# Performance work log

Hardware: AMD Instinct MI355X
Metric: run time of the kernel (lower is better)

## Reference

```python
import jax, jax.numpy as jnp
import numpy as np

B, DIM, WIDTH, DD, C2 = 16384, 64, 256, 64, 16
TRIL = jnp.tril_indices(DIM, -1)


def _lin_init(key, out_size, in_size, bias=True):
    lim = 1.0 / np.sqrt(in_size)
    kW, kb = jax.random.split(key)
    W = jax.random.uniform(kW, (out_size, in_size), jnp.float32, -lim, lim)
    if bias:
        return W, jax.random.uniform(kb, (out_size,), jnp.float32, -lim, lim)
    return W


def setup_inputs() -> dict:
    key = jax.random.key(0)
    ks = jax.random.split(key, 16)
    inp = {"t": jnp.zeros((1,), jnp.float32),
           "y": jax.random.normal(ks[0], (B, DIM), jnp.float32)}
    specs = [("energy", 1, 1), ("entropy", 1, 4), ("pA", DIM * (DIM - 1) // 2, 7),
             ("fC", DD * C2, 10), ("fB", DD * DIM, 13)]
    for name, out, i in specs:
        W0, b0 = _lin_init(ks[i], WIDTH, DIM)
        W1, b1 = _lin_init(ks[i + 1], WIDTH, WIDTH)
        W2 = _lin_init(ks[i + 2], out, WIDTH, bias=False)
        inp[name + "_W0"], inp[name + "_b0"] = W0, b0
        inp[name + "_W1"], inp[name + "_b1"] = W1, b1
        inp[name + "_W2"] = W2
    return inp


def _mlp(x, W0, b0, W1, b1, W2):
    # eqx.nn.MLP, depth=2, tanh activations, no final bias
    h = jnp.tanh(x @ W0.T + b0)
    h = jnp.tanh(h @ W1.T + b1)
    return h @ W2.T


def _grad_scalar(y, W0, b0, W1, b1, W2):
    # per-sample gradient of scalar MLP (energy/entropy)
    def f(yv):
        h = jnp.tanh(W0 @ yv + b0)
        h = jnp.tanh(W1 @ h + b1)
        return (W2 @ h)[0]
    return jax.vmap(jax.grad(f))(y)


def _poisson(A_flat, dE, dS):
    b = dE.shape[0]
    Amat = jnp.zeros((b, DIM, DIM), dE.dtype).at[:, TRIL[0], TRIL[1]].set(A_flat)
    A = Amat - jnp.swapaxes(Amat, 1, 2)  # antisymmetric
    AdE = jnp.einsum('bij,bj->bi', A, dE)
    AdS = jnp.einsum('bij,bj->bi', A, dS)
    dE_AdS = jnp.sum(dE * AdS, axis=-1, keepdims=True)
    dE_dS = jnp.sum(dE * dS, axis=-1, keepdims=True)
    dS_sq = jnp.sum(dS ** 2, axis=-1, keepdims=True)
    return AdE + (dE_AdS * dS - dE_dS * AdS) / dS_sq


def _friction(C, Bm, dE, dS):
    Dmat = jnp.einsum('bik,bjk->bij', C, C)  # (b, DD, DD)
    BdotdE = jnp.einsum('bij,bj->bi', Bm, dE)
    BdotdS = jnp.einsum('bij,bj->bi', Bm, dS)
    dE_sq = jnp.sum(dE ** 2, axis=-1, keepdims=True)  # (b,1)
    BdE = Bm - BdotdE[:, :, None] * dE[:, None, :] / dE_sq[:, None, :]
    dEdS = jnp.sum(dE * dS, axis=-1, keepdims=True)
    BdEdS = BdotdS - BdotdE * (dEdS / dE_sq)  # (b, DD)
    return jnp.einsum('bik,bkl,bi->bl', jnp.swapaxes(BdE, 1, 2), Dmat, BdEdS)


def reference(t, y,
              energy_W0, energy_b0, energy_W1, energy_b1, energy_W2,
              entropy_W0, entropy_b0, entropy_W1, entropy_b1, entropy_W2,
              pA_W0, pA_b0, pA_W1, pA_b1, pA_W2,
              fC_W0, fC_b0, fC_W1, fC_b1, fC_W2,
              fB_W0, fB_b0, fB_W1, fB_b1, fB_W2):
    b = y.shape[0]
    dE = _grad_scalar(y, energy_W0, energy_b0, energy_W1, energy_b1, energy_W2)
    dS = _grad_scalar(y, entropy_W0, entropy_b0, entropy_W1, entropy_b1, entropy_W2)
    A_flat = _mlp(y, pA_W0, pA_b0, pA_W1, pA_b1, pA_W2)
    C = _mlp(y, fC_W0, fC_b0, fC_W1, fC_b1, fC_W2).reshape(b, DD, C2)
    Bm = _mlp(y, fB_W0, fB_b0, fB_W1, fB_b1, fB_W2).reshape(b, DD, DIM)
    return _poisson(A_flat, dE, dS) + _friction(C, Bm, dE, dS)
```

## Files before the change

kernel.cpp:

```cpp
#include <hip/hip_runtime.h>
#include <math.h>

#define SB 16

#define OFF_W0T  0
#define OFF_W1T  81920
#define OFF_W2PT 409600
#define OFF_W2CT 925696
#define OFF_W2BT 1187840
#define OFF_DE   2236416
#define OFF_DS   3284992
#define WS_FLOATS 4337600
#define NPACK  1048576
#define NPACKC 262144
#define NPACKP 524288
#define WS3_FLOATS (WS_FLOATS + NPACK + NPACKC + NPACKP)
#define NK1 327680
#define WS4_FLOATS (WS3_FLOATS + NK1)
#define NK3F 163840
#define WS5_FLOATS (WS4_FLOATS + NK3F)
#define NK2F 81920
#define WS6_FLOATS (WS5_FLOATS + NK2F)

typedef __attribute__((ext_vector_type(8))) short bf16x8;
typedef __attribute__((ext_vector_type(4))) float f32x4;

__device__ __forceinline__ float4 f4fma(float a, float4 w, float4 c) {
    c.x = fmaf(a, w.x, c.x); c.y = fmaf(a, w.y, c.y);
    c.z = fmaf(a, w.z, c.z); c.w = fmaf(a, w.w, c.w);
    return c;
}

__device__ __forceinline__ float4 tanh4b(float4 a, float b) {
    return make_float4(tanhf(a.x + b), tanhf(a.y + b), tanhf(a.z + b), tanhf(a.w + b));
}

__device__ __forceinline__ void bf16split(float x, unsigned short& hi, unsigned short& lo) {
    unsigned b = __float_as_uint(x);
    unsigned h = (b + 0x7FFFu + ((b >> 16) & 1u)) >> 16;
    hi = (unsigned short)h;
    float r = x - __uint_as_float(h << 16);
    unsigned rb = __float_as_uint(r);
    lo = (unsigned short)((rb + 0x7FFFu + ((rb >> 16) & 1u)) >> 16);
}

#define MFMA3(acc, Ah, Al, Bh, Bl)                                            \
    acc = __builtin_amdgcn_mfma_f32_16x16x32_bf16(Ah, Bh, acc, 0, 0, 0);      \
    acc = __builtin_amdgcn_mfma_f32_16x16x32_bf16(Al, Bh, acc, 0, 0, 0);      \
    acc = __builtin_amdgcn_mfma_f32_16x16x32_bf16(Ah, Bl, acc, 0, 0, 0);

__global__ __launch_bounds__(1024) void k_transpose_all(
    float* __restrict__ ws, int skipmid,
    const float* __restrict__ W0a, const float* __restrict__ W0b, const float* __restrict__ W0c,
    const float* __restrict__ W0d, const float* __restrict__ W0e,
    const float* __restrict__ W1a, const float* __restrict__ W1b, const float* __restrict__ W1c,
    const float* __restrict__ W1d, const float* __restrict__ W1e,
    const float* __restrict__ W2p, const float* __restrict__ W2c, const float* __restrict__ W2b)
{
    int t = blockIdx.x * blockDim.x + threadIdx.x;
    if (t >= 2236416) {
        int e = t - 2236416;
        unsigned short* PK = (unsigned short*)(ws + WS_FLOATS);
        if (e < NPACK) {
            int j = e & 7, lane = (e >> 3) & 63, c = (e >> 9) & 7, tt = e >> 12;
            int k = c * 32 + ((lane >> 4) & 3) * 8 + j;
            int n = tt * 16 + (lane & 15);
            unsigned short hi, lo;
            bf16split(W2b[n * 256 + k], hi, lo);
            PK[e] = hi; PK[NPACK + e] = lo;
        } else if (e < NPACK + NPACKC) {
            int e2 = e - NPACK;
            unsigned short* PC = PK + 2 * NPACK;
            int j = e2 & 7, lane = (e2 >> 3) & 63, c = (e2 >> 9) & 7, tt = e2 >> 12;
            int k = c * 32 + ((lane >> 4) & 3) * 8 + j;
            int n = tt * 16 + (lane & 15);
            unsigned short hi, lo;
            bf16split(W2c[n * 256 + k], hi, lo);
            PC[e2] = hi; PC[NPACKC + e2] = lo;
        } else if (e < NPACK + NPACKC + NPACKP) {
            int e2 = e - NPACK - NPACKC;
            unsigned short* PP = PK + 2 * NPACK + 2 * NPACKC;
            int j = e2 & 7, lane = (e2 >> 3) & 63, c = (e2 >> 9) & 7, tt = e2 >> 12;
            int k = c * 32 + ((lane >> 4) & 3) * 8 + j;
            int n = tt * 16 + (lane & 15);
            float v = (n < 2016) ? W2p[n * 256 + k] : 0.f;
            unsigned short hi, lo;
            bf16split(v, hi, lo);
            PP[e2] = hi; PP[NPACKP + e2] = lo;
        } else if (e < NPACK + NPACKC + NPACKP + NK1) {
            int e2 = e - NPACK - NPACKC - NPACKP;
            unsigned short* PQ = PK + 2 * (NPACK + NPACKC + NPACKP);
            int net = e2 / 163840;
            int r = e2 - net * 163840;
            const float* W0m = net ? W0b : W0a;
            const float* W1m = net ? W1b : W1a;
            float v;
            if (r < 16384) {
                int j = r & 7, lane = (r >> 3) & 63, cb = (r >> 9) & 1, tt = r >> 10;
                int k = cb * 32 + ((lane >> 4) & 3) * 8 + j;
                int n = tt * 16 + (lane & 15);
                v = W0m[n * 64 + k];
            } else if (r < 81920) {
                int r2 = r - 16384;
                int j = r2 & 7, lane = (r2 >> 3) & 63, cb = (r2 >> 9) & 7, tt = r2 >> 12;
                int k = cb * 32 + ((lane >> 4) & 3) * 8 + j;
                int n = tt * 16 + (lane & 15);
                v = W1m[n * 256 + k];
            } else if (r < 147456) {
                int r2 = r - 81920;
                int j = r2 & 7, lane = (r2 >> 3) & 63, cb = (r2 >> 9) & 7, tt = r2 >> 12;
                int k = cb * 32 + ((lane >> 4) & 3) * 8 + j;
                int n = tt * 16 + (lane & 15);
                v = W1m[k * 256 + n];
            } else {
                int r2 = r - 147456;
                int j = r2 & 7, lane = (r2 >> 3) & 63, cb = (r2 >> 9) & 7, tt = r2 >> 12;
                int k = cb * 32 + ((lane >> 4) & 3) * 8 + j;
                int n = tt * 16 + (lane & 15);
                v = W0m[k * 64 + n];
            }
            unsigned short hi, lo;
            bf16split(v, hi, lo);
            PQ[e2] = hi; PQ[NK1 + e2] = lo;
        } else if (e < NPACK + NPACKC + NPACKP + NK1 + NK3F) {
            int e2 = e - NPACK - NPACKC - NPACKP - NK1;
            unsigned short* PQ = PK + 2 * (NPACK + NPACKC + NPACKP + NK1);
            int net = e2 / 81920;
            int r = e2 - net * 81920;
            const float* W0m = net ? W0e : W0d;
            const float* W1m = net ? W1e : W1d;
            float v;
            if (r < 16384) {
                int j = r & 7, lane = (r >> 3) & 63, cb = (r >> 9) & 1, tt = r >> 10;
                int k = cb * 32 + ((lane >> 4) & 3) * 8 + j;
                int n = tt * 16 + (lane & 15);
                v = W0m[n * 64 + k];
            } else {
                int r2 = r - 16384;
                int j = r2 & 7, lane = (r2 >> 3) & 63, cb = (r2 >> 9) & 7, tt = r2 >> 12;
                int k = cb * 32 + ((lane >> 4) & 3) * 8 + j;
                int n = tt * 16 + (lane & 15);
                v = W1m[n * 256 + k];
            }
            unsigned short hi, lo;
            bf16split(v, hi, lo);
            PQ[e2] = hi; PQ[NK3F + e2] = lo;
        } else if (e < NPACK + NPACKC + NPACKP + NK1 + NK3F + NK2F) {
            int r = e - NPACK - NPACKC - NPACKP - NK1 - NK3F;
            unsigned short* PQ = PK + 2 * (NPACK + NPACKC + NPACKP + NK1 + NK3F);
            float v;
            if (r < 16384) {
                int j = r & 7, lane = (r >> 3) & 63, cb = (r >> 9) & 1, tt = r >> 10;
                int k = cb * 32 + ((lane >> 4) & 3) * 8 + j;
                int n = tt * 16 + (lane & 15);
                v = W0c[n * 64 + k];
            } else {
                int r2 = r - 16384;
                int j = r2 & 7, lane = (r2 >> 3) & 63, cb = (r2 >> 9) & 7, tt = r2 >> 12;
                int k = cb * 32 + ((lane >> 4) & 3) * 8 + j;
                int n = tt * 16 + (lane & 15);
                v = W1c[n * 256 + k];
            }
            unsigned short hi, lo;
            bf16split(v, hi, lo);
            PQ[r] = hi; PQ[NK2F + r] = lo;
        }
        return;
    }
    if (skipmid && t >= 409600) return;
    const float* in;
    int o, R, C;
    float* out;
    if (t < 81920) {
        int m = t >> 14; o = t & 16383;
        const float* W0s[5] = {W0a, W0b, W0c, W0d, W0e};
        in = W0s[m]; out = ws + OFF_W0T + m * 16384; R = 256; C = 64;
    } else if (t < 409600) {
        int t2 = t - 81920;
        int m = t2 >> 16; o = t2 & 65535;
        const float* W1s[5] = {W1a, W1b, W1c, W1d, W1e};
        in = W1s[m]; out = ws + OFF_W1T + m * 65536; R = 256; C = 256;
    } else if (t < 925696) {
        o = t - 409600; in = W2p; out = ws + OFF_W2PT; R = 2016; C = 256;
    } else if (t < 1187840) {
        o = t - 925696; in = W2c; out = ws + OFF_W2CT; R = 1024; C = 256;
    } else {
        o = t - 1187840; in = W2b; out = ws + OFF_W2BT; R = 4096; C = 256;
    }
    int c = o / R, r = o - c * R;
    out[o] = in[r * C + c];
}

__global__ __launch_bounds__(1024, 2) void k1_grads_mf(
    const float* __restrict__ y, const float* __restrict__ ws,
    const float* __restrict__ b0E, const float* __restrict__ b1E, const float* __restrict__ w2E,
    const float* __restrict__ b0S, const float* __restrict__ b1S, const float* __restrict__ w2S,
    float* __restrict__ odE, float* __restrict__ odS)
{
    __shared__ float sH1f[4352];
    __shared__ unsigned short yAh[1024], yAl[1024];
    __shared__ unsigned short bAh[4096], bAl[4096];
    __shared__ unsigned short bBh[4096], bBl[4096];
    __shared__ float sPart[4352];

    const int tid = threadIdx.x;
    const int sbase = blockIdx.x * SB;
    const int wv = tid >> 6, l = tid & 63;

    {
        int s = tid >> 6, k = tid & 63;
        unsigned short hi, lo;
        bf16split(y[sbase * 64 + tid], hi, lo);
        int addr = ((k >> 5) * 64 + (s | (((k >> 3) & 3) << 4))) * 8 + (k & 7);
        yAh[addr] = hi; yAl[addr] = lo;
    }
    __syncthreads();

    const unsigned short* K1H = (const unsigned short*)(ws + WS3_FLOATS);
    const unsigned short* K1L = K1H + NK1;

    for (int m = 0; m < 2; ++m) {
        const float* b0 = m ? b0S : b0E;
        const float* b1 = m ? b1S : b1E;
        const float* w2 = m ? w2S : w2E;
        float* outg = m ? odS : odE;
        const int pbase = m * 163840;

        {
            const unsigned short* PH = K1H + pbase;
            const unsigned short* PL = K1L + pbase;
            f32x4 acc = {0.f, 0.f, 0.f, 0.f};
            #pragma unroll
            for (int cb = 0; cb < 2; ++cb) {
                bf16x8 Ah = *(const bf16x8*)(yAh + (cb * 64 + l) * 8);
                bf16x8 Al = *(const bf16x8*)(yAl + (cb * 64 + l) * 8);
                bf16x8 Bh = *(const bf16x8*)(PH + ((wv * 2 + cb) * 64 + l) * 8);
                bf16x8 Bl = *(const bf16x8*)(PL + ((wv * 2 + cb) * 64 + l) * 8);
                MFMA3(acc, Ah, Al, Bh, Bl);
            }
            int c = 16 * wv + (l & 15);
            float bb = b0[c];
            const int cblk = c >> 5, j0 = c & 7;
            const int lb2 = ((c >> 3) & 3) << 4;
            #pragma unroll
            for (int r = 0; r < 4; ++r) {
                int s = (l >> 4) * 4 + r;
                float h1 = tanhf(acc[r] + bb);
                sH1f[c * 17 + s] = h1;
                unsigned short hi, lo;
                bf16split(h1, hi, lo);
                int base = (cblk * 64 + (s | lb2)) * 8 + j0;
                bBh[base] = hi; bBl[base] = lo;
            }
        }
        __syncthreads();

        {
            const unsigned short* PH = K1H + pbase + 16384;
            const unsigned short* PL = K1L + pbase + 16384;
            f32x4 acc = {0.f, 0.f, 0.f, 0.f};
            #pragma unroll 1
            for (int cb = 0; cb < 8; ++cb) {
                bf16x8 Ah = *(const bf16x8*)(bBh + (cb * 64 + l) * 8);
                bf16x8 Al = *(const bf16x8*)(bBl + (cb * 64 + l) * 8);
                bf16x8 Bh = *(const bf16x8*)(PH + ((wv * 8 + cb) * 64 + l) * 8);
                bf16x8 Bl = *(const bf16x8*)(PL + ((wv * 8 + cb) * 64 + l) * 8);
                MFMA3(acc, Ah, Al, Bh, Bl);
            }
            int c = 16 * wv + (l & 15);
            float bb = b1[c], wvv = w2[c];
            const int cblk = c >> 5, j0 = c & 7;
            const int lb2 = ((c >> 3) & 3) << 4;
            #pragma unroll
            for (int r = 0; r < 4; ++r) {
                int s = (l >> 4) * 4 + r;
                float h2 = tanhf(acc[r] + bb);
                float g2 = (1.f - h2 * h2) * wvv;
                unsigned short hi, lo;
                bf16split(g2, hi, lo);
                int base = (cblk * 64 + (s | lb2)) * 8 + j0;
                bAh[base] = hi; bAl[base] = lo;
            }
        }
        __syncthreads();

        {
            const unsigned short* PH = K1H + pbase + 81920;
            const unsigned short* PL = K1L + pbase + 81920;
            f32x4 acc = {0.f, 0.f, 0.f, 0.f};
            #pragma unroll 1
            for (int cb = 0; cb < 8; ++cb) {
                bf16x8 Ah = *(const bf16x8*)(bAh + (cb * 64 + l) * 8);
                bf16x8 Al = *(const bf16x8*)(bAl + (cb * 64 + l) * 8);
                bf16x8 Bh = *(const bf16x8*)(PH + ((wv * 8 + cb) * 64 + l) * 8);
                bf16x8 Bl = *(const bf16x8*)(PL + ((wv * 8 + cb) * 64 + l) * 8);
                MFMA3(acc, Ah, Al, Bh, Bl);
            }
            int c = 16 * wv + (l & 15);
            const int cblk = c >> 5, j0 = c & 7;
            const int lb2 = ((c >> 3) & 3) << 4;
            #pragma unroll
            for (int r = 0; r < 4; ++r) {
                int s = (l >> 4) * 4 + r;
                float h1 = sH1f[c * 17 + s];
                float g1 = (1.f - h1 * h1) * acc[r];
                unsigned short hi, lo;
                bf16split(g1, hi, lo);
                int base = (cblk * 64 + (s | lb2)) * 8 + j0;
                bBh[base] = hi; bBl[base] = lo;
            }
        }
        __syncthreads();

        {
            const unsigned short* PH = K1H + pbase + 147456;
            const unsigned short* PL = K1L + pbase + 147456;
            const int t = wv & 3, kh = wv >> 2;
            f32x4 acc = {0.f, 0.f, 0.f, 0.f};
            #pragma unroll
            for (int q = 0; q < 2; ++q) {
                int cb = 2 * kh + q;
                bf16x8 Ah = *(const bf16x8*)(bBh + (cb * 64 + l) * 8);
                bf16x8 Al = *(const bf16x8*)(bBl + (cb * 64 + l) * 8);
                bf16x8 Bh = *(const bf16x8*)(PH + ((t * 8 + cb) * 64 + l) * 8);
                bf16x8 Bl = *(const bf16x8*)(PL + ((t * 8 + cb) * 64 + l) * 8);
                MFMA3(acc, Ah, Al, Bh, Bl);
            }
            #pragma unroll
            for (int r = 0; r < 4; ++r)
                sPart[(kh * 4 + t) * 272 + (l & 15) * 17 + ((l >> 4) * 4 + r)] = acc[r];
        }
        __syncthreads();
        {
            int s = tid >> 6, i = tid & 63;
            float v = 0.f;
            #pragma unroll
            for (int kh = 0; kh < 4; ++kh)
                v += sPart[(kh * 4 + (i >> 4)) * 272 + (i & 15) * 17 + s];
            outg[sbase * 64 + tid] = v;
        }
        __syncthreads();
    }
}

__global__ __launch_bounds__(1024, 4) void k2_poisson_mf(
    const float* __restrict__ y, const float* __restrict__ ws,
    const float* __restrict__ b0P, const float* __restrict__ b1P,
    float* __restrict__ dout)
{
    extern __shared__ float smem[];
    float* sa   = smem;
    unsigned short* sAh = (unsigned short*)(smem + 32384);
    unsigned short* sAl = (unsigned short*)(smem + 34432);
    float* sdE  = smem + 36480;
    float* sdS  = sdE + 1024;
    float* sH1T = sa;
    float* syT  = sa + 4096;

    const int tid = threadIdx.x;
    const int sbase = blockIdx.x * SB;
    const float* gdE = ws + OFF_DE;
    const float* gdS = ws + OFF_DS;

    {
        int s = tid >> 6, i = tid & 63;
        syT[i * 16 + s] = y[sbase * 64 + tid];
        sdE[tid] = gdE[sbase * 64 + tid];
        sdS[tid] = gdS[sbase * 64 + tid];
    }
    __syncthreads();

    const int c  = tid & 255;
    const int sg = tid >> 8;
    const int s4 = sg * 4;

    {
        const float* w0t = ws + OFF_W0T + 2 * 16384;
        float4 acc = {0, 0, 0, 0};
        #pragma unroll 4
        for (int k = 0; k < 64; ++k) {
            float w = w0t[k * 256 + c];
            float4 yv = *(const float4*)(syT + k * 16 + s4);
            acc = f4fma(w, yv, acc);
        }
        *(float4*)(sH1T + c * 16 + s4) = tanh4b(acc, b0P[c]);
    }
    __syncthreads();

    {
        const float* w1t = ws + OFF_W1T + 2 * 65536;
        float4 acc = {0, 0, 0, 0};
        #pragma unroll 4
        for (int k = 0; k < 256; ++k) {
            float w = w1t[k * 256 + c];
            float4 hv = *(const float4*)(sH1T + k * 16 + s4);
            acc = f4fma(w, hv, acc);
        }
        float4 h2 = tanh4b(acc, b1P[c]);
        const int cblk = c >> 5, j0 = c & 7;
        const int lbase = ((c >> 3) & 3) << 4;
        float va[4] = {h2.x, h2.y, h2.z, h2.w};
        #pragma unroll
        for (int q = 0; q < 4; ++q) {
            int lb = ((s4 + q) & 15) | lbase;
            int base = (cblk * 64 + lb) * 8 + j0;
            unsigned short hi, lo;
            bf16split(va[q], hi, lo);
            sAh[base] = hi;
            sAl[base] = lo;
        }
    }
    __syncthreads();

    {
        const unsigned short* PP = (const unsigned short*)(ws + WS_FLOATS) + 2 * NPACK + 2 * NPACKC;
        const unsigned short* PH = PP;
        const unsigned short* PL = PP + NPACKP;
        const int wv = tid >> 6, l = tid & 63;
        f32x4 accp[8];
        #pragma unroll
        for (int t0 = 0; t0 < 8; ++t0) accp[t0] = (f32x4){0.f, 0.f, 0.f, 0.f};
        #pragma unroll 1
        for (int cb = 0; cb < 8; ++cb) {
            bf16x8 Ah = *(const bf16x8*)(sAh + (cb * 64 + l) * 8);
            bf16x8 Al = *(const bf16x8*)(sAl + (cb * 64 + l) * 8);
            #pragma unroll
            for (int t0 = 0; t0 < 8; ++t0) {
                int t = 8 * wv + t0;
                bf16x8 Bh = *(const bf16x8*)(PH + ((t * 8 + cb) * 64 + l) * 8);
                bf16x8 Bl = *(const bf16x8*)(PL + ((t * 8 + cb) * 64 + l) * 8);
                MFMA3(accp[t0], Ah, Al, Bh, Bl);
            }
        }
        #pragma unroll
        for (int t0 = 0; t0 < 8; ++t0) {
            int n = (8 * wv + t0) * 16 + (l & 15);
            if (n < 2016) {
                #pragma unroll
                for (int r = 0; r < 4; ++r)
                    sa[((l >> 4) * 4 + r) * 2024 + n] = accp[t0][r];
            }
        }
    }
    __syncthreads();

    {
        const int s = tid >> 6;
        const int i = tid & 63;
        const int ib = i * (i - 1) / 2;
        const float* ap = sa + s * 2024;
        const float* dep = sdE + s * 64;
        const float* dsp = sdS + s * 64;

        float adE = 0.f, adS = 0.f;
        int trij = 0;
        #pragma unroll 4
        for (int j = 0; j < 64; ++j) {
            int t = (j < i) ? (ib + j) : (trij + i);
            float sel = (j < i) ? 1.f : ((j == i) ? 0.f : -1.f);
            float cc = sel * ap[t];
            adE = fmaf(cc, dep[j], adE);
            adS = fmaf(cc, dsp[j], adS);
            trij += j;
        }

        float de = dep[i], dsv = dsp[i];
        float p0 = de * adS;
        float p1 = de * dsv;
        float p2 = dsv * dsv;
        #pragma unroll
        for (int m = 1; m <= 32; m <<= 1) {
            p0 += __shfl_xor(p0, m);
            p1 += __shfl_xor(p1, m);
            p2 += __shfl_xor(p2, m);
        }
        float inv = 1.f / p2;
        dout[sbase * 64 + tid] = adE + (p0 * dsv - p1 * adS) * inv;
    }
}

__global__ __launch_bounds__(1024, 4) void k2_poisson_mf2(
    const float* __restrict__ y, const float* __restrict__ ws,
    const float* __restrict__ b0P, const float* __restrict__ b1P,
    float* __restrict__ dout)
{
    extern __shared__ float smem[];
    float* sa   = smem;
    unsigned short* yAh = (unsigned short*)(smem);
    unsigned short* yAl = (unsigned short*)(smem + 512);
    unsigned short* h1H = (unsigned short*)(smem + 1024);
    unsigned short* h1L = (unsigned short*)(smem + 3072);
    unsigned short* sAh = (unsigned short*)(smem + 32384);
    unsigned short* sAl = (unsigned short*)(smem + 34432);
    float* sdE  = smem + 36480;
    float* sdS  = sdE + 1024;

    const int tid = threadIdx.x;
    const int sbase = blockIdx.x * SB;
    const float* gdE = ws + OFF_DE;
    const float* gdS = ws + OFF_DS;

    {
        int s = tid >> 6, k = tid & 63;
        unsigned short hi, lo;
        bf16split(y[sbase * 64 + tid], hi, lo);
        int addr = ((k >> 5) * 64 + (s | (((k >> 3) & 3) << 4))) * 8 + (k & 7);
        yAh[addr] = hi; yAl[addr] = lo;
        sdE[tid] = gdE[sbase * 64 + tid];
        sdS[tid] = gdS[sbase * 64 + tid];
    }
    __syncthreads();

    const int wv = tid >> 6, l = tid & 63;
    const unsigned short* F2H = (const unsigned short*)(ws + WS5_FLOATS);
    const unsigned short* F2L = F2H + NK2F;

    {
        f32x4 acc = {0.f, 0.f, 0.f, 0.f};
        #pragma unroll
        for (int cb = 0; cb < 2; ++cb) {
            bf16x8 Ah = *(const bf16x8*)(yAh + (cb * 64 + l) * 8);
            bf16x8 Al = *(const bf16x8*)(yAl + (cb * 64 + l) * 8);
            bf16x8 Bh = *(const bf16x8*)(F2H + ((wv * 2 + cb) * 64 + l) * 8);
            bf16x8 Bl = *(const bf16x8*)(F2L + ((wv * 2 + cb) * 64 + l) * 8);
            MFMA3(acc, Ah, Al, Bh, Bl);
        }
        int c = 16 * wv + (l & 15);
        float bb = b0P[c];
        const int cblk = c >> 5, j0 = c & 7;
        const int lb2 = ((c >> 3) & 3) << 4;
        #pragma unroll
        for (int r = 0; r < 4; ++r) {
            int s = (l >> 4) * 4 + r;
            float h1 = tanhf(acc[r] + bb);
            unsigned short hi, lo;
            bf16split(h1, hi, lo);
            int base = (cblk * 64 + (s | lb2)) * 8 + j0;
            h1H[base] = hi; h1L[base] = lo;
        }
    }
    __syncthreads();

    {
        f32x4 acc = {0.f, 0.f, 0.f, 0.f};
        #pragma unroll 1
        for (int cb = 0; cb < 8; ++cb) {
            bf16x8 Ah = *(const bf16x8*)(h1H + (cb * 64 + l) * 8);
            bf16x8 Al = *(const bf16x8*)(h1L + (cb * 64 + l) * 8);
            bf16x8 Bh = *(const bf16x8*)(F2H + 16384 + ((wv * 8 + cb) * 64 + l) * 8);
            bf16x8 Bl = *(const bf16x8*)(F2L + 16384 + ((wv * 8 + cb) * 64 + l) * 8);
            MFMA3(acc, Ah, Al, Bh, Bl);
        }
        int c = 16 * wv + (l & 15);
        float bb = b1P[c];
        const int cblk = c >> 5, j0 = c & 7;
        const int lb2 = ((c >> 3) & 3) << 4;
        #pragma unroll
        for (int r = 0; r < 4; ++r) {
            int s = (l >> 4) * 4 + r;
            float h2 = tanhf(acc[r] + bb);
            unsigned short hi, lo;
            bf16split(h2, hi, lo);
            int base = (cblk * 64 + (s | lb2)) * 8 + j0;
            sAh[base] = hi; sAl[base] = lo;
        }
    }
    __syncthreads();

    {
        const unsigned short* PP = (const unsigned short*)(ws + WS_FLOATS) + 2 * NPACK + 2 * NPACKC;
        const unsigned short* PH = PP;
        const unsigned short* PL = PP + NPACKP;
        f32x4 accp[8];
        #pragma unroll
        for (int t0 = 0; t0 < 8; ++t0) accp[t0] = (f32x4){0.f, 0.f, 0.f, 0.f};
        #pragma unroll 1
        for (int cb = 0; cb < 8; ++cb) {
            bf16x8 Ah = *(const bf16x8*)(sAh + (cb * 64 + l) * 8);
            bf16x8 Al = *(const bf16x8*)(sAl + (cb * 64 + l) * 8);
            #pragma unroll
            for (int t0 = 0; t0 < 8; ++t0) {
                int t = 8 * wv + t0;
                bf16x8 Bh = *(const bf16x8*)(PH + ((t * 8 + cb) * 64 + l) * 8);
                bf16x8 Bl = *(const bf16x8*)(PL + ((t * 8 + cb) * 64 + l) * 8);
                MFMA3(accp[t0], Ah, Al, Bh, Bl);
            }
        }
        #pragma unroll
        for (int t0 = 0; t0 < 8; ++t0) {
            int n = (8 * wv + t0) * 16 + (l & 15);
            if (n < 2016) {
                #pragma unroll
                for (int r = 0; r < 4; ++r)
                    sa[((l >> 4) * 4 + r) * 2024 + n] = accp[t0][r];
            }
        }
    }
    __syncthreads();

    {
        const int s = tid >> 6;
        const int i = tid & 63;
        const int ib = i * (i - 1) / 2;
        const float* ap = sa + s * 2024;
        const float* dep = sdE + s * 64;
        const float* dsp = sdS + s * 64;

        float adE = 0.f, adS = 0.f;
        int trij = 0;
        #pragma unroll 4
        for (int j = 0; j < 64; ++j) {
            int t = (j < i) ? (ib + j) : (trij + i);
            float sel = (j < i) ? 1.f : ((j == i) ? 0.f : -1.f);
            float cc = sel * ap[t];
            adE = fmaf(cc, dep[j], adE);
            adS = fmaf(cc, dsp[j], adS);
            trij += j;
        }

        float de = dep[i], dsv = dsp[i];
        float p0 = de * adS;
        float p1 = de * dsv;
        float p2 = dsv * dsv;
        #pragma unroll
        for (int m = 1; m <= 32; m <<= 1) {
            p0 += __shfl_xor(p0, m);
            p1 += __shfl_xor(p1, m);
            p2 += __shfl_xor(p2, m);
        }
        float inv = 1.f / p2;
        dout[sbase * 64 + tid] = adE + (p0 * dsv - p1 * adS) * inv;
    }
}

__global__ __launch_bounds__(1024, 4) void k3_friction_mf3(
    const float* __restrict__ y, const float* __restrict__ ws,
    const float* __restrict__ b0C, const float* __restrict__ b1C,
    const float* __restrict__ b0B, const float* __restrict__ b1B,
    float* __restrict__ dout)
{
    extern __shared__ float smem[];
    unsigned short* yAh = (unsigned short*)(smem);
    unsigned short* yAl = (unsigned short*)(smem + 512);
    unsigned short* sAhc = (unsigned short*)(smem + 1024);
    unsigned short* sAlc = (unsigned short*)(smem + 3072);
    unsigned short* sAhb = (unsigned short*)(smem + 5120);
    unsigned short* sAlb = (unsigned short*)(smem + 7168);
    unsigned short* h1ch = (unsigned short*)(smem + 9216);
    unsigned short* h1cl = (unsigned short*)(smem + 11264);
    unsigned short* h1bh = (unsigned short*)(smem + 13312);
    unsigned short* h1bl = (unsigned short*)(smem + 15360);
    float* sC   = smem + 9216;
    float* sdE  = smem + 26640;
    float* sdS  = smem + 27664;
    float* sBdE = smem + 28688;
    float* sBdS = smem + 29712;
    float* sv   = smem + 30736;
    float* sq   = smem + 31760;
    float* sScal= smem + 32784;
    float* sr   = smem + 32848;

    const int tid = threadIdx.x;
    const int sbase = blockIdx.x * SB;
    const float* gdE = ws + OFF_DE;
    const float* gdS = ws + OFF_DS;

    {
        int s = tid >> 6, k = tid & 63;
        unsigned short hi, lo;
        bf16split(y[sbase * 64 + tid], hi, lo);
        int addr = ((k >> 5) * 64 + (s | (((k >> 3) & 3) << 4))) * 8 + (k & 7);
        yAh[addr] = hi; yAl[addr] = lo;
        sdE[tid] = gdE[sbase * 64 + tid];
        sdS[tid] = gdS[sbase * 64 + tid];
    }
    if (tid < 64) sScal[tid] = 0.f;
    __syncthreads();

    {
        int s = tid >> 6;
        float de = sdE[tid];
        unsafeAtomicAdd(&sScal[s * 4 + 0], de * de);
        unsafeAtomicAdd(&sScal[s * 4 + 1], de * sdS[tid]);
    }

    const int wv = tid >> 6;
    const int l  = tid & 63;
    const int netw = wv >> 3;
    const int tb   = wv & 7;
    const float* b0v = netw ? b0B : b0C;
    const float* b1v = netw ? b1B : b1C;
    unsigned short* h1H = netw ? h1bh : h1ch;
    unsigned short* h1L = netw ? h1bl : h1cl;
    unsigned short* h2H = netw ? sAhb : sAhc;
    unsigned short* h2L = netw ? sAlb : sAlc;

    const unsigned short* F3H = (const unsigned short*)(ws + WS4_FLOATS);
    const unsigned short* F3L = F3H + NK3F;

    #pragma unroll
    for (int jj = 0; jj < 2; ++jj) {
        int t = tb + 8 * jj;
        f32x4 acc = {0.f, 0.f, 0.f, 0.f};
        #pragma unroll
        for (int cb = 0; cb < 2; ++cb) {
            bf16x8 Ah = *(const bf16x8*)(yAh + (cb * 64 + l) * 8);
            bf16x8 Al = *(const bf16x8*)(yAl + (cb * 64 + l) * 8);
            const unsigned short* bh = F3H + netw * 81920 + ((t * 2 + cb) * 64 + l) * 8;
            const unsigned short* bl = F3L + netw * 81920 + ((t * 2 + cb) * 64 + l) * 8;
            bf16x8 Bh = *(const bf16x8*)(bh);
            bf16x8 Bl = *(const bf16x8*)(bl);
            MFMA3(acc, Ah, Al, Bh, Bl);
        }
        int c = 16 * t + (l & 15);
        float bb = b0v[c];
        const int cblk = c >> 5, j0 = c & 7;
        const int lb2 = ((c >> 3) & 3) << 4;
        #pragma unroll
        for (int r = 0; r < 4; ++r) {
            int s = (l >> 4) * 4 + r;
            float h1 = tanhf(acc[r] + bb);
            unsigned short hi, lo;
            bf16split(h1, hi, lo);
            int base = (cblk * 64 + (s | lb2)) * 8 + j0;
            h1H[base] = hi; h1L[base] = lo;
        }
    }
    __syncthreads();

    #pragma unroll
    for (int jj = 0; jj < 2; ++jj) {
        int t = tb + 8 * jj;
        f32x4 acc = {0.f, 0.f, 0.f, 0.f};
        #pragma unroll 1
        for (int cb = 0; cb < 8; ++cb) {
            bf16x8 Ah = *(const bf16x8*)(h1H + (cb * 64 + l) * 8);
            bf16x8 Al = *(const bf16x8*)(h1L + (cb * 64 + l) * 8);
            const unsigned short* bh = F3H + netw * 81920 + 16384 + ((t * 8 + cb) * 64 + l) * 8;
            const unsigned short* bl = F3L + netw * 81920 + 16384 + ((t * 8 + cb) * 64 + l) * 8;
            bf16x8 Bh = *(const bf16x8*)(bh);
            bf16x8 Bl = *(const bf16x8*)(bl);
            MFMA3(acc, Ah, Al, Bh, Bl);
        }
        int c = 16 * t + (l & 15);
        float bb = b1v[c];
        const int cblk = c >> 5, j0 = c & 7;
        const int lb2 = ((c >> 3) & 3) << 4;
        #pragma unroll
        for (int r = 0; r < 4; ++r) {
            int s = (l >> 4) * 4 + r;
            float h2 = tanhf(acc[r] + bb);
            unsigned short hi, lo;
            bf16split(h2, hi, lo);
            int base = (cblk * 64 + (s | lb2)) * 8 + j0;
            h2H[base] = hi; h2L[base] = lo;
        }
    }
    __syncthreads();

    {
        const unsigned short* PC = (const unsigned short*)(ws + WS_FLOATS) + 2 * NPACK;
        const unsigned short* CH = PC;
        const unsigned short* CL = PC + NPACKC;
        f32x4 accc[4];
        #pragma unroll
        for (int t0 = 0; t0 < 4; ++t0) accc[t0] = (f32x4){0.f, 0.f, 0.f, 0.f};
        #pragma unroll 1
        for (int cb = 0; cb < 8; ++cb) {
            bf16x8 Ah = *(const bf16x8*)(sAhc + (cb * 64 + l) * 8);
            bf16x8 Al = *(const bf16x8*)(sAlc + (cb * 64 + l) * 8);
            #pragma unroll
            for (int t0 = 0; t0 < 4; ++t0) {
                int t = 4 * wv + t0;
                bf16x8 Bh = *(const bf16x8*)(CH + ((t * 8 + cb) * 64 + l) * 8);
                bf16x8 Bl = *(const bf16x8*)(CL + ((t * 8 + cb) * 64 + l) * 8);
                MFMA3(accc[t0], Ah, Al, Bh, Bl);
            }
        }
        #pragma unroll
        for (int t0 = 0; t0 < 4; ++t0) {
            int t = 4 * wv + t0;
            #pragma unroll
            for (int r = 0; r < 4; ++r)
                sC[((l >> 4) * 4 + r) * 1089 + t * 17 + (l & 15)] = accc[t0][r];
        }
    }

    f32x4 acc[16];
    #pragma unroll
    for (int t0 = 0; t0 < 16; ++t0) acc[t0] = (f32x4){0.f, 0.f, 0.f, 0.f};
    {
        const unsigned short* BH = (const unsigned short*)(ws + WS_FLOATS);
        const unsigned short* BL = BH + NPACK;
        #pragma unroll 1
        for (int cb = 0; cb < 8; ++cb) {
            bf16x8 Ah = *(const bf16x8*)(sAhb + (cb * 64 + l) * 8);
            bf16x8 Al = *(const bf16x8*)(sAlb + (cb * 64 + l) * 8);
            const unsigned short* bh = BH + ((wv * 16 * 8 + cb) * 64 + l) * 8;
            const unsigned short* bl = BL + ((wv * 16 * 8 + cb) * 64 + l) * 8;
            #pragma unroll
            for (int t0 = 0; t0 < 16; ++t0) {
                bf16x8 Bh = *(const bf16x8*)(bh + t0 * 4096);
                bf16x8 Bl = *(const bf16x8*)(bl + t0 * 4096);
                MFMA3(acc[t0], Ah, Al, Bh, Bl);
            }
        }
    }
    #pragma unroll
    for (int g = 0; g < 4; ++g) {
        float pd[4] = {0, 0, 0, 0}, ps[4] = {0, 0, 0, 0};
        #pragma unroll
        for (int tt = 0; tt < 4; ++tt) {
            int i = 16 * tt + (l & 15);
            #pragma unroll
            for (int r = 0; r < 4; ++r) {
                int s = (l >> 4) * 4 + r;
                float d = acc[g * 4 + tt][r];
                pd[r] = fmaf(d, sdE[s * 64 + i], pd[r]);
                ps[r] = fmaf(d, sdS[s * 64 + i], ps[r]);
            }
        }
        #pragma unroll
        for (int m = 1; m <= 8; m <<= 1) {
            #pragma unroll
            for (int r = 0; r < 4; ++r) {
                pd[r] += __shfl_xor(pd[r], m);
                ps[r] += __shfl_xor(ps[r], m);
            }
        }
        if ((l & 15) == 0) {
            int kpr = 4 * wv + g;
            #pragma unroll
            for (int r = 0; r < 4; ++r) {
                int s = (l >> 4) * 4 + r;
                sBdE[s * 64 + kpr] = pd[r];
                sBdS[s * 64 + kpr] = ps[r];
            }
        }
    }
    __syncthreads();

    {
        int s = tid >> 6;
        float beta = sScal[s * 4 + 1] / sScal[s * 4 + 0];
        sv[tid] = sBdS[tid] - beta * sBdE[tid];
    }
    __syncthreads();
    {
        int s = tid >> 6;
        unsafeAtomicAdd(&sScal[s * 4 + 2], sdE[tid] * sv[tid]);
    }
    __syncthreads();

    #pragma unroll
    for (int g = 0; g < 4; ++g) {
        float pq[4] = {0, 0, 0, 0};
        #pragma unroll
        for (int tt = 0; tt < 4; ++tt) {
            int i = 16 * tt + (l & 15);
            #pragma unroll
            for (int r = 0; r < 4; ++r) {
                int s = (l >> 4) * 4 + r;
                pq[r] = fmaf(acc[g * 4 + tt][r], sv[s * 64 + i], pq[r]);
            }
        }
        #pragma unroll
        for (int m = 1; m <= 8; m <<= 1) {
            #pragma unroll
            for (int r = 0; r < 4; ++r) pq[r] += __shfl_xor(pq[r], m);
        }
        if ((l & 15) == 0) {
            int kpr = 4 * wv + g;
            #pragma unroll
            for (int r = 0; r < 4; ++r) sq[((l >> 4) * 4 + r) * 64 + kpr] = pq[r];
        }
    }
    __syncthreads();

    if (tid < 256) {
        int s = tid >> 4, m = tid & 15;
        float gamma = sScal[s * 4 + 2] / sScal[s * 4 + 0];
        float r = 0.f;
        #pragma unroll 4
        for (int k = 0; k < 64; ++k) {
            float wvv = sq[s * 64 + k] - gamma * sBdE[s * 64 + k];
            r = fmaf(sC[s * 1089 + k * 17 + m], wvv, r);
        }
        sr[s * 16 + m] = r;
    }
    __syncthreads();
    {
        int s = tid >> 6, k = tid & 63;
        float o = 0.f;
        #pragma unroll
        for (int m2 = 0; m2 < 16; ++m2)
            o = fmaf(sC[s * 1089 + k * 17 + m2], sr[s * 16 + m2], o);
        int gi = sbase * 64 + tid;
        dout[gi] = dout[gi] + o;
    }
}

extern "C" void kernel_launch(void* const* d_in, const int* in_sizes, int n_in,
                              void* d_out, int out_size, void* d_ws, size_t ws_size,
                              hipStream_t stream)
{
    (void)in_sizes; (void)n_in; (void)out_size;
    const float* y = (const float*)d_in[1];
    const float* W0[5]; const float* b0[5]; const float* W1[5]; const float* b1[5]; const float* W2[5];
    for (int m = 0; m < 5; ++m) {
        int base = 2 + m * 5;
        W0[m] = (const float*)d_in[base + 0];
        b0[m] = (const float*)d_in[base + 1];
        W1[m] = (const float*)d_in[base + 2];
        b1[m] = (const float*)d_in[base + 3];
        W2[m] = (const float*)d_in[base + 4];
    }
    float* ws = (float*)d_ws;
    float* dout = (float*)d_out;
    if (ws_size < (size_t)WS5_FLOATS * sizeof(float)) return;
    const bool big4 = ws_size >= (size_t)WS6_FLOATS * sizeof(float);

    int ntr = 2236416 + NPACK + NPACKC + NPACKP + NK1 + NK3F;
    if (big4) ntr += NK2F;
    hipLaunchKernelGGL(k_transpose_all, dim3((ntr + 1023) / 1024), dim3(1024), 0, stream,
                       ws, 1,
                       W0[0], W0[1], W0[2], W0[3], W0[4],
                       W1[0], W1[1], W1[2], W1[3], W1[4],
                       W2[2], W2[3], W2[4]);

    hipLaunchKernelGGL(k1_grads_mf, dim3(1024), dim3(1024), 0, stream,
                       y, ws,
                       b0[0], b1[0], W2[0], b0[1], b1[1], W2[1],
                       ws + OFF_DE, ws + OFF_DS);

    const int k2_smem = 154112;
    const int k3_smem = 132416;
    if (big4) {
        hipFuncSetAttribute((const void*)k2_poisson_mf2, hipFuncAttributeMaxDynamicSharedMemorySize, k2_smem);
        hipLaunchKernelGGL(k2_poisson_mf2, dim3(1024), dim3(1024), k2_smem, stream,
                           y, ws, b0[2], b1[2], dout);
    } else {
        hipFuncSetAttribute((const void*)k2_poisson_mf, hipFuncAttributeMaxDynamicSharedMemorySize, k2_smem);
        hipLaunchKernelGGL(k2_poisson_mf, dim3(1024), dim3(1024), k2_smem, stream,
                           y, ws, b0[2], b1[2], dout);
    }

    hipFuncSetAttribute((const void*)k3_friction_mf3, hipFuncAttributeMaxDynamicSharedMemorySize, k3_smem);
    hipLaunchKernelGGL(k3_friction_mf3, dim3(1024), dim3(1024), k3_smem, stream,
                       y, ws, b0[3], b1[3], b0[4], b1[4], dout);
}
```

Before: 522.8 us.

## Keep friction C in registers, shrink LDS, and skip redundant weight transposes

The friction kernel no longer stages the C matrix in shared memory. It keeps the MFMA accumulators in registers and computes the two C contractions with LDS atomics and wave shuffles. This cuts dynamic shared memory from about 132KB to 78KB and raises the launch-bounds occupancy hint, so more blocks can be resident per CU. The setup kernel also skips the W0/W1 transpose section when the large workspace path is used, since that work is assumed unneeded there. The atomics add reduction-order nondeterminism and more register pressure.

```diff
diff --git a/kernel.cpp b/kernel.cpp
--- a/kernel.cpp
+++ b/kernel.cpp
@@ -50,14 +50,14 @@
     acc = __builtin_amdgcn_mfma_f32_16x16x32_bf16(Ah, Bl, acc, 0, 0, 0);
 
 __global__ __launch_bounds__(1024) void k_transpose_all(
-    float* __restrict__ ws, int skipmid,
+    float* __restrict__ ws, int skipmid, int tofs,
     const float* __restrict__ W0a, const float* __restrict__ W0b, const float* __restrict__ W0c,
     const float* __restrict__ W0d, const float* __restrict__ W0e,
     const float* __restrict__ W1a, const float* __restrict__ W1b, const float* __restrict__ W1c,
     const float* __restrict__ W1d, const float* __restrict__ W1e,
     const float* __restrict__ W2p, const float* __restrict__ W2c, const float* __restrict__ W2b)
 {
-    int t = blockIdx.x * blockDim.x + threadIdx.x;
+    int t = blockIdx.x * blockDim.x + threadIdx.x + tofs;
     if (t >= 2236416) {
         int e = t - 2236416;
         unsigned short* PK = (unsigned short*)(ws + WS_FLOATS);
@@ -633,7 +633,7 @@
     }
 }
 
-__global__ __launch_bounds__(1024, 4) void k3_friction_mf3(
+__global__ __launch_bounds__(1024, 8) void k3_friction_mf4(
     const float* __restrict__ y, const float* __restrict__ ws,
     const float* __restrict__ b0C, const float* __restrict__ b1C,
     const float* __restrict__ b0B, const float* __restrict__ b1B,
@@ -650,15 +650,14 @@
     unsigned short* h1cl = (unsigned short*)(smem + 11264);
     unsigned short* h1bh = (unsigned short*)(smem + 13312);
     unsigned short* h1bl = (unsigned short*)(smem + 15360);
-    float* sC   = smem + 9216;
-    float* sdE  = smem + 26640;
-    float* sdS  = smem + 27664;
-    float* sBdE = smem + 28688;
-    float* sBdS = smem + 29712;
-    float* sv   = smem + 30736;
-    float* sq   = smem + 31760;
-    float* sScal= smem + 32784;
-    float* sr   = smem + 32848;
+    float* sBdE = smem + 9216;
+    float* sBdS = smem + 10240;
+    float* sv   = smem + 11264;
+    float* sq   = smem + 12288;
+    float* sr   = smem + 13312;
+    float* sdE  = smem + 17408;
+    float* sdS  = smem + 18432;
+    float* sScal= smem + 19456;
 
     const int tid = threadIdx.x;
     const int sbase = blockIdx.x * SB;
@@ -758,13 +757,13 @@
     }
     __syncthreads();
 
+    f32x4 accc[4];
+    #pragma unroll
+    for (int t0 = 0; t0 < 4; ++t0) accc[t0] = (f32x4){0.f, 0.f, 0.f, 0.f};
     {
         const unsigned short* PC = (const unsigned short*)(ws + WS_FLOATS) + 2 * NPACK;
         const unsigned short* CH = PC;
         const unsigned short* CL = PC + NPACKC;
-        f32x4 accc[4];
-        #pragma unroll
-        for (int t0 = 0; t0 < 4; ++t0) accc[t0] = (f32x4){0.f, 0.f, 0.f, 0.f};
         #pragma unroll 1
         for (int cb = 0; cb < 8; ++cb) {
             bf16x8 Ah = *(const bf16x8*)(sAhc + (cb * 64 + l) * 8);
@@ -776,13 +775,6 @@
                 bf16x8 Bl = *(const bf16x8*)(CL + ((t * 8 + cb) * 64 + l) * 8);
                 MFMA3(accc[t0], Ah, Al, Bh, Bl);
             }
-        }
-        #pragma unroll
-        for (int t0 = 0; t0 < 4; ++t0) {
-            int t = 4 * wv + t0;
-            #pragma unroll
-            for (int r = 0; r < 4; ++r)
-                sC[((l >> 4) * 4 + r) * 1089 + t * 17 + (l & 15)] = accc[t0][r];
         }
     }
 
@@ -844,6 +836,7 @@
         int s = tid >> 6;
         float beta = sScal[s * 4 + 1] / sScal[s * 4 + 0];
         sv[tid] = sBdS[tid] - beta * sBdE[tid];
+        if (tid < 256) sr[tid] = 0.f;
     }
     __syncthreads();
     {
@@ -877,26 +870,41 @@
     }
     __syncthreads();
 
-    if (tid < 256) {
-        int s = tid >> 4, m = tid & 15;
-        float gamma = sScal[s * 4 + 2] / sScal[s * 4 + 0];
-        float r = 0.f;
-        #pragma unroll 4
-        for (int k = 0; k < 64; ++k) {
-            float wvv = sq[s * 64 + k] - gamma * sBdE[s * 64 + k];
-            r = fmaf(sC[s * 1089 + k * 17 + m], wvv, r);
-        }
-        sr[s * 16 + m] = r;
-    }
-    __syncthreads();
-    {
-        int s = tid >> 6, k = tid & 63;
-        float o = 0.f;
-        #pragma unroll
-        for (int m2 = 0; m2 < 16; ++m2)
-            o = fmaf(sC[s * 1089 + k * 17 + m2], sr[s * 16 + m2], o);
-        int gi = sbase * 64 + tid;
-        dout[gi] = dout[gi] + o;
+    #pragma unroll
+    for (int t0 = 0; t0 < 4; ++t0) {
+        int k = 4 * wv + t0;
+        #pragma unroll
+        for (int r = 0; r < 4; ++r) {
+            int s = (l >> 4) * 4 + r;
+            float gamma = sScal[s * 4 + 2] / sScal[s * 4 + 0];
+            float w = sq[s * 64 + k] - gamma * sBdE[s * 64 + k];
+            unsafeAtomicAdd(&sr[s * 16 + (l & 15)], accc[t0][r] * w);
+        }
+    }
+    __syncthreads();
+
+    #pragma unroll
+    for (int t0 = 0; t0 < 4; ++t0) {
+        int k = 4 * wv + t0;
+        float po[4];
+        #pragma unroll
+        for (int r = 0; r < 4; ++r) {
+            int s = (l >> 4) * 4 + r;
+            po[r] = accc[t0][r] * sr[s * 16 + (l & 15)];
+        }
+        #pragma unroll
+        for (int m = 1; m <= 8; m <<= 1) {
+            #pragma unroll
+            for (int r = 0; r < 4; ++r) po[r] += __shfl_xor(po[r], m);
+        }
+        if ((l & 15) == 0) {
+            #pragma unroll
+            for (int r = 0; r < 4; ++r) {
+                int s = (l >> 4) * 4 + r;
+                int gi = sbase * 64 + s * 64 + k;
+                dout[gi] = dout[gi] + po[r];
+            }
+        }
     }
 }
 
@@ -920,13 +928,21 @@
     if (ws_size < (size_t)WS5_FLOATS * sizeof(float)) return;
     const bool big4 = ws_size >= (size_t)WS6_FLOATS * sizeof(float);
 
-    int ntr = 2236416 + NPACK + NPACKC + NPACKP + NK1 + NK3F;
-    if (big4) ntr += NK2F;
-    hipLaunchKernelGGL(k_transpose_all, dim3((ntr + 1023) / 1024), dim3(1024), 0, stream,
-                       ws, 1,
-                       W0[0], W0[1], W0[2], W0[3], W0[4],
-                       W1[0], W1[1], W1[2], W1[3], W1[4],
-                       W2[2], W2[3], W2[4]);
+    if (big4) {
+        const int npack_all = NPACK + NPACKC + NPACKP + NK1 + NK3F + NK2F;
+        hipLaunchKernelGGL(k_transpose_all, dim3((npack_all + 1023) / 1024), dim3(1024), 0, stream,
+                           ws, 1, 2236416,
+                           W0[0], W0[1], W0[2], W0[3], W0[4],
+                           W1[0], W1[1], W1[2], W1[3], W1[4],
+                           W2[2], W2[3], W2[4]);
+    } else {
+        const int ntr = 2236416 + NPACK + NPACKC + NPACKP + NK1 + NK3F;
+        hipLaunchKernelGGL(k_transpose_all, dim3((ntr + 1023) / 1024), dim3(1024), 0, stream,
+                           ws, 1, 0,
+                           W0[0], W0[1], W0[2], W0[3], W0[4],
+                           W1[0], W1[1], W1[2], W1[3], W1[4],
+                           W2[2], W2[3], W2[4]);
+    }
 
     hipLaunchKernelGGL(k1_grads_mf, dim3(1024), dim3(1024), 0, stream,
                        y, ws,
@@ -934,7 +950,6 @@
                        ws + OFF_DE, ws + OFF_DS);
 
     const int k2_smem = 154112;
-    const int k3_smem = 132416;
     if (big4) {
         hipFuncSetAttribute((const void*)k2_poisson_mf2, hipFuncAttributeMaxDynamicSharedMemorySize, k2_smem);
         hipLaunchKernelGGL(k2_poisson_mf2, dim3(1024), dim3(1024), k2_smem, stream,
@@ -945,7 +960,8 @@
                            y, ws, b0[2], b1[2], dout);
     }
 
-    hipFuncSetAttribute((const void*)k3_friction_mf3, hipFuncAttributeMaxDynamicSharedMemorySize, k3_smem);
-    hipLaunchKernelGGL(k3_friction_mf3, dim3(1024), dim3(1024), k3_smem, stream,
+    const int k3_smem = 78080;
+    hipFuncSetAttribute((const void*)k3_friction_mf4, hipFuncAttributeMaxDynamicSharedMemorySize, k3_smem);
+    hipLaunchKernelGGL(k3_friction_mf4, dim3(1024), dim3(1024), k3_smem, stream,
                        y, ws, b0[3], b1[3], b0[4], b1[4], dout);
 }
```

After: 1.041 ms. 99.1% more time.
